# Optimization experiments

Hardware: AMD Instinct MI355X
Metric: run time of the kernel (lower is better)

The kernel has to match this reference:

```python
import jax, jax.numpy as jnp
import numpy as np
import math

COARSE_K = 20
FINE_K = 10
KNOWLEDGE_RANK = 128


def setup_inputs() -> dict:
    key = jax.random.key(0)
    ks = jax.random.split(key, 5)
    B, S, D = 2, 2048, 1024
    NK = 65536
    return {
        "x": jax.random.normal(ks[0], (B, S, D), dtype=jnp.float32),
        "W_router": jax.random.normal(ks[1], (D, NK), dtype=jnp.float32) * 0.02,
        "W_enc": jax.random.normal(ks[2], (D, KNOWLEDGE_RANK), dtype=jnp.float32) * 0.02,
        "K_all": jax.random.normal(ks[3], (NK, KNOWLEDGE_RANK), dtype=jnp.float32) * 0.02,
        "V_all": jax.random.normal(ks[4], (NK, D), dtype=jnp.float32) * 0.02,
    }


def reference(x, W_router, W_enc, K_all, V_all):
    # Stage 1: coarse routing over full knowledge table
    k_logits = jnp.einsum('bsd,dn->bsn', x, W_router)          # [B,S,NK]
    coarse_scores, candidate_idx = jax.lax.top_k(k_logits, COARSE_K)  # [B,S,Ck]

    # Stage 2: fine scoring against gathered coarse candidates
    query = jnp.einsum('bsd,dr->bsr', x, W_enc)                # [B,S,R]
    K_candidates = K_all[candidate_idx]                        # [B,S,Ck,R]
    fine_scores = jnp.einsum('bsr,bscr->bsc', query, K_candidates) / math.sqrt(KNOWLEDGE_RANK)

    fine_topk_scores, fine_local_idx = jax.lax.top_k(fine_scores, FINE_K)  # [B,S,Fk]
    fine_weights = jax.nn.softmax(fine_topk_scores, axis=-1)
    fine_global_idx = jnp.take_along_axis(candidate_idx, fine_local_idx, axis=-1)  # [B,S,Fk]

    selected_V = V_all[fine_global_idx]                        # [B,S,Fk,D]
    output = jnp.einsum('bsfd,bsf->bsd', selected_V, fine_weights)
    return output
```

## Files before the change

kernel.cpp:

```cpp
#include <hip/hip_runtime.h>

#define DIM 1024
#define NKN 65536
#define TOK 4096
#define CK 20
#define FK 10
#define RNK 128
#define CAP 256
#define NCHUNK 512

typedef __bf16 v8bf __attribute__((ext_vector_type(8)));
typedef float v4f __attribute__((ext_vector_type(4)));

#define AS1 __attribute__((address_space(1)))
#define AS3 __attribute__((address_space(3)))

__device__ __forceinline__ unsigned short f2bf(float f) {
  unsigned u = __builtin_bit_cast(unsigned, f);
  u += 0x7FFFu + ((u >> 16) & 1u);
  return (unsigned short)(u >> 16);
}
__device__ __forceinline__ unsigned short bf2key(unsigned short b) {
  return (b & 0x8000) ? (unsigned short)(~b) : (unsigned short)(b | 0x8000);
}

__global__ __launch_bounds__(256) void k_transpose(const float* __restrict__ W,
                                                   float* __restrict__ WT,
                                                   unsigned short* __restrict__ WTb) {
  __shared__ float tile[32][33];
  const int n0 = (blockIdx.x & 2047) << 5;
  const int d0 = (blockIdx.x >> 11) << 5;
  const int c = threadIdx.x & 31, r0 = threadIdx.x >> 5;
#pragma unroll
  for (int i = 0; i < 4; i++) {
    int r = r0 + i * 8;
    tile[r][c] = W[(size_t)(d0 + r) * NKN + n0 + c];
  }
  __syncthreads();
#pragma unroll
  for (int i = 0; i < 4; i++) {
    int r = r0 + i * 8;
    float v = tile[c][r];
    size_t o = (size_t)(n0 + r) * DIM + d0 + c;
    WT[o] = v;
    WTb[o] = f2bf(v);
  }
}

__global__ __launch_bounds__(256) void k_cvt_x(const float* __restrict__ x,
                                               unsigned short* __restrict__ xb) {
  const int i = blockIdx.x * 256 + threadIdx.x;
  const float4 v = reinterpret_cast<const float4*>(x)[i];
  ushort4 o;
  o.x = f2bf(v.x); o.y = f2bf(v.y); o.z = f2bf(v.z); o.w = f2bf(v.w);
  reinterpret_cast<ushort4*>(xb)[i] = o;
}

__global__ __launch_bounds__(512, 4) void k_gemm(const unsigned short* __restrict__ A,
                                                 const unsigned short* __restrict__ Bt,
                                                 unsigned short* __restrict__ Lg,
                                                 unsigned short* __restrict__ CmaxT) {
  __shared__ __align__(16) char lds[73728];
  const int tid = threadIdx.x;
  const int lane = tid & 63, wid = tid >> 6;
  const int wm = wid >> 1, wn = wid & 1;
  const int mb = blockIdx.x & 15, nb = blockIdx.x >> 4;
  const int m0 = mb << 8, n0 = nb << 7;
  const int rm = lane & 15, lq = lane >> 4;
  v4f acc[4][4] = {};

  const int u8 = (((tid & 3) ^ ((tid >> 3) & 3)) << 3);
  const unsigned short* aSrc = A + (size_t)(m0 + (tid >> 2)) * DIM + u8;
  const unsigned short* bSrc = Bt + (size_t)(n0 + (tid >> 2)) * DIM + u8;

  const int sx = ((lq ^ ((rm >> 1) & 3)) << 4);
  const int aOff = (wm * 64 + rm) * 64 + sx;
  const int bOff = 16384 + (wn * 64 + rm) * 64 + sx;

#define STAGE(SLOT, KT) do { \
    char* _b = lds + (SLOT) * 24576 + tid * 16; \
    __builtin_amdgcn_global_load_lds((const AS1 void*)(aSrc + (KT)),             (AS3 void*)(_b),         16, 0, 0); \
    __builtin_amdgcn_global_load_lds((const AS1 void*)(aSrc + (KT) + 128 * DIM), (AS3 void*)(_b + 8192),  16, 0, 0); \
    __builtin_amdgcn_global_load_lds((const AS1 void*)(bSrc + (KT)),             (AS3 void*)(_b + 16384), 16, 0, 0); \
  } while (0)

#define TILE(T, VM, DOSTAGE) do { \
    if (DOSTAGE) STAGE(((T) + 2) % 3, ((T) + 2) * 32); \
    asm volatile("s_waitcnt vmcnt(" VM ")" ::: "memory"); \
    __builtin_amdgcn_s_barrier(); \
    const char* sb = lds + ((T) % 3) * 24576; \
    v8bf a0 = *(const v8bf*)(sb + aOff); \
    v8bf a1 = *(const v8bf*)(sb + aOff + 1024); \
    v8bf a2 = *(const v8bf*)(sb + aOff + 2048); \
    v8bf a3 = *(const v8bf*)(sb + aOff + 3072); \
    v8bf b0 = *(const v8bf*)(sb + bOff); \
    v8bf b1 = *(const v8bf*)(sb + bOff + 1024); \
    v8bf b2 = *(const v8bf*)(sb + bOff + 2048); \
    v8bf b3 = *(const v8bf*)(sb + bOff + 3072); \
    __builtin_amdgcn_s_setprio(1); \
    _Pragma("unroll") for (int nf = 0; nf < 4; ++nf) { \
      v8bf bb = (nf == 0) ? b0 : (nf == 1) ? b1 : (nf == 2) ? b2 : b3; \
      acc[0][nf] = __builtin_amdgcn_mfma_f32_16x16x32_bf16(a0, bb, acc[0][nf], 0, 0, 0); \
      acc[1][nf] = __builtin_amdgcn_mfma_f32_16x16x32_bf16(a1, bb, acc[1][nf], 0, 0, 0); \
      acc[2][nf] = __builtin_amdgcn_mfma_f32_16x16x32_bf16(a2, bb, acc[2][nf], 0, 0, 0); \
      acc[3][nf] = __builtin_amdgcn_mfma_f32_16x16x32_bf16(a3, bb, acc[3][nf], 0, 0, 0); \
    } \
    __builtin_amdgcn_s_setprio(0); \
    __builtin_amdgcn_s_barrier(); \
  } while (0)

  STAGE(0, 0);
  STAGE(1, 32);

  for (int t = 0; t < 30; ++t) {
    TILE(t, "6", true);
  }
  TILE(30, "3", false);
  TILE(31, "0", false);
#undef TILE
#undef STAGE

  const int mr = lq * 4;
  float rmax[4][4];
#pragma unroll
  for (int fr = 0; fr < 4; ++fr) {
#pragma unroll
    for (int r = 0; r < 4; ++r) {
      float mx = acc[fr][0][r];
#pragma unroll
      for (int nf = 1; nf < 4; ++nf) mx = fmaxf(mx, acc[fr][nf][r]);
      rmax[fr][r] = mx;
    }
#pragma unroll
    for (int nf = 0; nf < 4; ++nf) {
      const int mrow = m0 + wm * 64 + fr * 16 + mr;
      const int ncol = n0 + wn * 64 + nf * 16 + rm;
#pragma unroll
      for (int r = 0; r < 4; ++r)
        Lg[(size_t)(mrow + r) * NKN + ncol] = f2bf(acc[fr][nf][r]);
    }
  }
#pragma unroll
  for (int fr = 0; fr < 4; ++fr)
#pragma unroll
    for (int r = 0; r < 4; ++r) {
#pragma unroll
      for (int off = 1; off < 16; off <<= 1)
        rmax[fr][r] = fmaxf(rmax[fr][r], __shfl_xor(rmax[fr][r], off));
    }
  __syncthreads();
  float* smax = (float*)lds;
  if (rm == 0) {
#pragma unroll
    for (int fr = 0; fr < 4; ++fr)
#pragma unroll
      for (int r = 0; r < 4; ++r)
        smax[wn * 256 + wm * 64 + fr * 16 + mr + r] = rmax[fr][r];
  }
  __syncthreads();
  if (tid < 256) {
    float v = fmaxf(smax[tid], smax[256 + tid]);
    CmaxT[(size_t)nb * TOK + m0 + tid] = bf2key(f2bf(v));
  }
}

__global__ __launch_bounds__(256) void k_pick(const unsigned short* __restrict__ CmaxT,
                                              const unsigned short* __restrict__ Lg,
                                              int* __restrict__ cidx,
                                              int* __restrict__ ccnt) {
  __shared__ unsigned short keys[NCHUNK];
  __shared__ int qlist[NCHUNK];
  __shared__ int qn, scnt, bsS;
  const int t = blockIdx.x, tid = threadIdx.x;
  const int lane = tid & 63, w = tid >> 6;
  keys[tid] = CmaxT[(size_t)tid * TOK + t];
  keys[tid + 256] = CmaxT[(size_t)(tid + 256) * TOK + t];
  if (tid == 0) { qn = 0; scnt = 0; }
  __syncthreads();
  if (w == 0) {
    int v[8];
#pragma unroll
    for (int j = 0; j < 8; j++) v[j] = keys[lane * 8 + j];
    int t32 = 0;
    for (int it = 0; it < 32; it++) {
      int lm = v[0];
#pragma unroll
      for (int j = 1; j < 8; j++) lm = max(lm, v[j]);
      int gm = lm;
#pragma unroll
      for (int off = 32; off > 0; off >>= 1) gm = max(gm, __shfl_xor(gm, off));
      unsigned long long msk = __ballot(lm == gm);
      if (lane == __ffsll((long long)msk) - 1) {
        bool done = false;
#pragma unroll
        for (int j = 0; j < 8; j++)
          if (!done && v[j] == gm) { v[j] = -1; done = true; }
      }
      t32 = gm;
    }
    if (lane == 0) bsS = t32;
  }
  __syncthreads();
  const int bs = bsS;
  for (int c = tid; c < NCHUNK; c += 256)
    if ((int)keys[c] >= bs) { int p = atomicAdd(&qn, 1); qlist[p] = c; }
  __syncthreads();
  const int nq = qn;
  const int sub = tid >> 7, e = tid & 127;
  for (int qi = sub; qi < nq; qi += 2) {
    const int col = qlist[qi] * 128 + e;
    unsigned short key = bf2key(Lg[(size_t)t * NKN + col]);
    if ((int)key >= bs) {
      int p = atomicAdd(&scnt, 1);
      if (p < CAP) cidx[(size_t)t * CAP + p] = col;
    }
  }
  __syncthreads();
  if (tid == 0) ccnt[t] = min(scnt, CAP);
}

__global__ __launch_bounds__(256) void k_rescore(const float* __restrict__ x,
                                                 const float* __restrict__ WT,
                                                 const int* __restrict__ cidx,
                                                 const int* __restrict__ ccnt,
                                                 int* __restrict__ coarse) {
  __shared__ float xs[DIM];
  __shared__ double sc[CAP];
  __shared__ int ci[CAP];
  const int t = blockIdx.x, tid = threadIdx.x;
  const int lane = tid & 63, w = tid >> 6;
  const int cnt = ccnt[t];
  for (int i = tid; i < DIM; i += 256) xs[i] = x[(size_t)t * DIM + i];
  for (int i = tid; i < CAP; i += 256) {
    sc[i] = -1e300;
    ci[i] = (i < cnt) ? cidx[(size_t)t * CAP + i] : 0;
  }
  __syncthreads();
  for (int c = w; c < cnt; c += 4) {
    const float* wr = WT + (size_t)ci[c] * DIM;
    double sacc = 0.0;
#pragma unroll 4
    for (int i = lane; i < DIM; i += 64) sacc += (double)xs[i] * (double)wr[i];
#pragma unroll
    for (int off = 32; off > 0; off >>= 1) sacc += __shfl_down(sacc, off);
    if (lane == 0) sc[c] = sacc;
  }
  __syncthreads();
  if (w == 0) {
    double v[4];
    int ix[4];
#pragma unroll
    for (int j = 0; j < 4; j++) { v[j] = sc[lane + j * 64]; ix[j] = lane + j * 64; }
    for (int kk = 0; kk < CK; kk++) {
      double v1 = v[0]; int i1 = ix[0];
#pragma unroll
      for (int j = 1; j < 4; j++)
        if (v[j] > v1) { v1 = v[j]; i1 = ix[j]; }
#pragma unroll
      for (int off = 32; off > 0; off >>= 1) {
        double ov = __shfl_down(v1, off);
        int oi = __shfl_down(i1, off);
        if (ov > v1) { v1 = ov; i1 = oi; }
      }
      i1 = __shfl(i1, 0);
      if (lane == 0) coarse[(size_t)t * CK + kk] = ci[i1];
#pragma unroll
      for (int j = 0; j < 4; j++)
        if (i1 == ix[j]) v[j] = -1e300;
    }
  }
}

__global__ __launch_bounds__(128) void k_query(const float* __restrict__ x,
                                               const float* __restrict__ Wenc,
                                               float* __restrict__ q) {
  const int j = threadIdx.x;
  const int t0 = blockIdx.x * 4;
  float s0 = 0.f, s1 = 0.f, s2 = 0.f, s3 = 0.f;
  const float* x0 = x + (size_t)t0 * DIM;
  for (int d = 0; d < DIM; d++) {
    float wv = Wenc[d * RNK + j];
    s0 = fmaf(x0[d], wv, s0);
    s1 = fmaf(x0[DIM + d], wv, s1);
    s2 = fmaf(x0[2 * DIM + d], wv, s2);
    s3 = fmaf(x0[3 * DIM + d], wv, s3);
  }
  q[(size_t)t0 * RNK + j] = s0;
  q[(size_t)(t0 + 1) * RNK + j] = s1;
  q[(size_t)(t0 + 2) * RNK + j] = s2;
  q[(size_t)(t0 + 3) * RNK + j] = s3;
}

__global__ __launch_bounds__(256) void k_fine(const float* __restrict__ q,
                                              const float* __restrict__ Kall,
                                              const float* __restrict__ Vall,
                                              const int* __restrict__ coarse,
                                              float* __restrict__ out) {
  __shared__ float qs[RNK];
  __shared__ float fsc[CK];
  __shared__ int gix[CK];
  __shared__ float wts[FK];
  __shared__ int fidx[FK];
  const int t = blockIdx.x, tid = threadIdx.x;
  const int lane = tid & 63, w = tid >> 6;
  if (tid < RNK) qs[tid] = q[(size_t)t * RNK + tid];
  if (tid < CK) gix[tid] = coarse[(size_t)t * CK + tid];
  __syncthreads();
  for (int c = w; c < CK; c += 4) {
    const float* kr = Kall + (size_t)gix[c] * RNK;
    float s = 0.f;
    s = fmaf(qs[lane], kr[lane], s);
    s = fmaf(qs[lane + 64], kr[lane + 64], s);
#pragma unroll
    for (int off = 32; off > 0; off >>= 1) s += __shfl_down(s, off);
    if (lane == 0) fsc[c] = s * 0.08838834764831843f;
  }
  __syncthreads();
  if (w == 0) {
    float vv = (lane < CK) ? fsc[lane] : -3e38f;
    float myv = -3e38f; int myp = 0;
    for (int kk = 0; kk < FK; kk++) {
      float v1 = vv; int p1 = lane;
#pragma unroll
      for (int off = 32; off > 0; off >>= 1) {
        float ov = __shfl_down(v1, off);
        int op = __shfl_down(p1, off);
        if (ov > v1) { v1 = ov; p1 = op; }
      }
      v1 = __shfl(v1, 0); p1 = __shfl(p1, 0);
      if (lane == kk) { myv = v1; myp = p1; }
      if (lane == p1) vv = -3e38f;
    }
    float sv = (lane < FK) ? myv : -3e38f;
    float mx = sv;
#pragma unroll
    for (int off = 8; off > 0; off >>= 1) mx = fmaxf(mx, __shfl_xor(mx, off, 16));
    float e = (lane < FK) ? expf(sv - mx) : 0.f;
    float se = e;
#pragma unroll
    for (int off = 8; off > 0; off >>= 1) se += __shfl_xor(se, off, 16);
    if (lane < FK) { wts[lane] = e / se; fidx[lane] = gix[myp]; }
  }
  __syncthreads();
  float4 a = make_float4(0.f, 0.f, 0.f, 0.f);
#pragma unroll
  for (int f = 0; f < FK; f++) {
    const float wt = wts[f];
    const float4 v = *reinterpret_cast<const float4*>(&Vall[(size_t)fidx[f] * DIM + tid * 4]);
    a.x = fmaf(wt, v.x, a.x);
    a.y = fmaf(wt, v.y, a.y);
    a.z = fmaf(wt, v.z, a.z);
    a.w = fmaf(wt, v.w, a.w);
  }
  *reinterpret_cast<float4*>(&out[(size_t)t * DIM + tid * 4]) = a;
}


extern "C" void kernel_launch(void* const* d_in, const int* in_sizes, int n_in,
                              void* d_out, int out_size, void* d_ws, size_t ws_size,
                              hipStream_t stream) {
  const float* x = (const float*)d_in[0];
  const float* Wr = (const float*)d_in[1];
  const float* Wenc = (const float*)d_in[2];
  const float* Kall = (const float*)d_in[3];
  const float* Vall = (const float*)d_in[4];
  float* out = (float*)d_out;

  char* ws = (char*)d_ws;
  constexpr size_t OFF_WT = 0;
  constexpr size_t OFF_WTB = 268435456;
  constexpr size_t OFF_XB = 402653184;
  constexpr size_t OFF_LG = 411041792;
  constexpr size_t OFF_CMAX = 947912704;
  float* WT = (float*)(ws + OFF_WT);
  unsigned short* WTb = (unsigned short*)(ws + OFF_WTB);
  unsigned short* xb = (unsigned short*)(ws + OFF_XB);
  unsigned short* Lg = (unsigned short*)(ws + OFF_LG);
  unsigned short* CmaxT = (unsigned short*)(ws + OFF_CMAX);
  int* cidx = (int*)(ws + OFF_XB);
  int* ccnt = (int*)(ws + OFF_XB + 4194304);
  int* coarse = (int*)(ws + OFF_XB + 4259840);
  float* q = (float*)(ws + OFF_WTB);

  k_transpose<<<65536, 256, 0, stream>>>(Wr, WT, WTb);
  k_cvt_x<<<4096, 256, 0, stream>>>(x, xb);
  k_gemm<<<8192, 512, 0, stream>>>(xb, WTb, Lg, CmaxT);
  k_pick<<<4096, 256, 0, stream>>>(CmaxT, Lg, cidx, ccnt);
  k_rescore<<<4096, 256, 0, stream>>>(x, WT, cidx, ccnt, coarse);
  k_query<<<1024, 128, 0, stream>>>(x, Wenc, q);
  k_fine<<<4096, 256, 0, stream>>>(q, Kall, Vall, coarse, out);
}
```

Baseline: 1.045 ms.

## Fuse pick with rescore and query with fine; use nontemporal stores

Merges the candidate-pick and fp64 rescore kernels so candidate indices stay in shared memory instead of going through global buffers. The query projection now runs inside the fine kernel, with each block computing its token's 128-dim query from x and W_enc. The transposed weight and logits stores become nontemporal to reduce cache pollution. Per-token query recomputation reads W_enc once per block, which adds memory traffic compared with the batched query kernel.

```diff
diff --git a/kernel.cpp b/kernel.cpp
--- a/kernel.cpp
+++ b/kernel.cpp
@@ -42,7 +42,7 @@
     int r = r0 + i * 8;
     float v = tile[c][r];
     size_t o = (size_t)(n0 + r) * DIM + d0 + c;
-    WT[o] = v;
+    __builtin_nontemporal_store(v, &WT[o]);
     WTb[o] = f2bf(v);
   }
 }
@@ -137,7 +137,8 @@
       const int ncol = n0 + wn * 64 + nf * 16 + rm;
 #pragma unroll
       for (int r = 0; r < 4; ++r)
-        Lg[(size_t)(mrow + r) * NKN + ncol] = f2bf(acc[fr][nf][r]);
+        __builtin_nontemporal_store(f2bf(acc[fr][nf][r]),
+                                    &Lg[(size_t)(mrow + r) * NKN + ncol]);
     }
   }
 #pragma unroll
@@ -164,17 +165,22 @@
   }
 }
 
-__global__ __launch_bounds__(256) void k_pick(const unsigned short* __restrict__ CmaxT,
-                                              const unsigned short* __restrict__ Lg,
-                                              int* __restrict__ cidx,
-                                              int* __restrict__ ccnt) {
+__global__ __launch_bounds__(256) void k_pickscore(const unsigned short* __restrict__ CmaxT,
+                                                   const unsigned short* __restrict__ Lg,
+                                                   const float* __restrict__ x,
+                                                   const float* __restrict__ WT,
+                                                   int* __restrict__ coarse) {
   __shared__ unsigned short keys[NCHUNK];
   __shared__ int qlist[NCHUNK];
+  __shared__ float xs[DIM];
+  __shared__ double sc[CAP];
+  __shared__ int ci[CAP];
   __shared__ int qn, scnt, bsS;
   const int t = blockIdx.x, tid = threadIdx.x;
   const int lane = tid & 63, w = tid >> 6;
   keys[tid] = CmaxT[(size_t)tid * TOK + t];
   keys[tid + 256] = CmaxT[(size_t)(tid + 256) * TOK + t];
+  for (int i = tid; i < DIM; i += 256) xs[i] = x[(size_t)t * DIM + i];
   if (tid == 0) { qn = 0; scnt = 0; }
   __syncthreads();
   if (w == 0) {
@@ -212,29 +218,14 @@
     unsigned short key = bf2key(Lg[(size_t)t * NKN + col]);
     if ((int)key >= bs) {
       int p = atomicAdd(&scnt, 1);
-      if (p < CAP) cidx[(size_t)t * CAP + p] = col;
-    }
-  }
-  __syncthreads();
-  if (tid == 0) ccnt[t] = min(scnt, CAP);
-}
-
-__global__ __launch_bounds__(256) void k_rescore(const float* __restrict__ x,
-                                                 const float* __restrict__ WT,
-                                                 const int* __restrict__ cidx,
-                                                 const int* __restrict__ ccnt,
-                                                 int* __restrict__ coarse) {
-  __shared__ float xs[DIM];
-  __shared__ double sc[CAP];
-  __shared__ int ci[CAP];
-  const int t = blockIdx.x, tid = threadIdx.x;
-  const int lane = tid & 63, w = tid >> 6;
-  const int cnt = ccnt[t];
-  for (int i = tid; i < DIM; i += 256) xs[i] = x[(size_t)t * DIM + i];
-  for (int i = tid; i < CAP; i += 256) {
-    sc[i] = -1e300;
-    ci[i] = (i < cnt) ? cidx[(size_t)t * CAP + i] : 0;
-  }
+      if (p < CAP) ci[p] = col;
+    }
+  }
+  __syncthreads();
+  const int cnt = min(scnt, CAP);
+  for (int i = tid; i < CAP; i += 256)
+    if (i >= cnt) ci[i] = 0;
+  for (int i = tid; i < CAP; i += 256) sc[i] = -1e300;
   __syncthreads();
   for (int c = w; c < cnt; c += 4) {
     const float* wr = WT + (size_t)ci[c] * DIM;
@@ -271,31 +262,14 @@
   }
 }
 
-__global__ __launch_bounds__(128) void k_query(const float* __restrict__ x,
-                                               const float* __restrict__ Wenc,
-                                               float* __restrict__ q) {
-  const int j = threadIdx.x;
-  const int t0 = blockIdx.x * 4;
-  float s0 = 0.f, s1 = 0.f, s2 = 0.f, s3 = 0.f;
-  const float* x0 = x + (size_t)t0 * DIM;
-  for (int d = 0; d < DIM; d++) {
-    float wv = Wenc[d * RNK + j];
-    s0 = fmaf(x0[d], wv, s0);
-    s1 = fmaf(x0[DIM + d], wv, s1);
-    s2 = fmaf(x0[2 * DIM + d], wv, s2);
-    s3 = fmaf(x0[3 * DIM + d], wv, s3);
-  }
-  q[(size_t)t0 * RNK + j] = s0;
-  q[(size_t)(t0 + 1) * RNK + j] = s1;
-  q[(size_t)(t0 + 2) * RNK + j] = s2;
-  q[(size_t)(t0 + 3) * RNK + j] = s3;
-}
-
-__global__ __launch_bounds__(256) void k_fine(const float* __restrict__ q,
+__global__ __launch_bounds__(256) void k_fine(const float* __restrict__ x,
+                                              const float* __restrict__ Wenc,
                                               const float* __restrict__ Kall,
                                               const float* __restrict__ Vall,
                                               const int* __restrict__ coarse,
                                               float* __restrict__ out) {
+  __shared__ float xs[DIM];
+  __shared__ float pq[2][RNK];
   __shared__ float qs[RNK];
   __shared__ float fsc[CK];
   __shared__ int gix[CK];
@@ -303,8 +277,20 @@
   __shared__ int fidx[FK];
   const int t = blockIdx.x, tid = threadIdx.x;
   const int lane = tid & 63, w = tid >> 6;
-  if (tid < RNK) qs[tid] = q[(size_t)t * RNK + tid];
+  reinterpret_cast<float4*>(xs)[tid] = reinterpret_cast<const float4*>(x + (size_t)t * DIM)[tid];
   if (tid < CK) gix[tid] = coarse[(size_t)t * CK + tid];
+  __syncthreads();
+  {
+    const int j = tid & 127, half = tid >> 7;
+    float s = 0.f;
+    const int d0 = half * 512;
+#pragma unroll 8
+    for (int d = 0; d < 512; d++)
+      s = fmaf(xs[d0 + d], Wenc[(size_t)(d0 + d) * RNK + j], s);
+    pq[half][j] = s;
+  }
+  __syncthreads();
+  if (tid < RNK) qs[tid] = pq[0][tid] + pq[1][tid];
   __syncthreads();
   for (int c = w; c < CK; c += 4) {
     const float* kr = Kall + (size_t)gix[c] * RNK;
@@ -377,16 +363,11 @@
   unsigned short* xb = (unsigned short*)(ws + OFF_XB);
   unsigned short* Lg = (unsigned short*)(ws + OFF_LG);
   unsigned short* CmaxT = (unsigned short*)(ws + OFF_CMAX);
-  int* cidx = (int*)(ws + OFF_XB);
-  int* ccnt = (int*)(ws + OFF_XB + 4194304);
-  int* coarse = (int*)(ws + OFF_XB + 4259840);
-  float* q = (float*)(ws + OFF_WTB);
+  int* coarse = (int*)(ws + OFF_XB);
 
   k_transpose<<<65536, 256, 0, stream>>>(Wr, WT, WTb);
   k_cvt_x<<<4096, 256, 0, stream>>>(x, xb);
   k_gemm<<<8192, 512, 0, stream>>>(xb, WTb, Lg, CmaxT);
-  k_pick<<<4096, 256, 0, stream>>>(CmaxT, Lg, cidx, ccnt);
-  k_rescore<<<4096, 256, 0, stream>>>(x, WT, cidx, ccnt, coarse);
-  k_query<<<1024, 128, 0, stream>>>(x, Wenc, q);
-  k_fine<<<4096, 256, 0, stream>>>(q, Kall, Vall, coarse, out);
-}
+  k_pickscore<<<4096, 256, 0, stream>>>(CmaxT, Lg, x, WT, coarse);
+  k_fine<<<4096, 256, 0, stream>>>(x, Wenc, Kall, Vall, coarse, out);
+}
```

Result: slower. 1.169 ms (+11.9%).
